# Optimization experiments

Measured on AMD Instinct MI355X. Metric: run time of the kernel, lower is better.

Reference implementation:

```python
import jax, jax.numpy as jnp
import numpy as np

DECAY = 0.99
EPS = 1e-05


def setup_inputs() -> dict:
    key = jax.random.key(0)
    k1, k2, k3, k4 = jax.random.split(key, 4)
    B, D, T, E = 16, 64, 4096, 1024
    x = jax.random.normal(k1, (B, D, T), dtype=jnp.float32)
    embedding = jax.random.uniform(k2, (E, D), dtype=jnp.float32,
                                   minval=-1.0 / E, maxval=1.0 / E)
    ema_size = jax.random.uniform(k3, (E,), dtype=jnp.float32)
    ema_w = jax.random.normal(k4, (D, E), dtype=jnp.float32)
    return {"x": x, "embedding": embedding, "ema_size": ema_size, "ema_w": ema_w}


def reference(x, embedding, ema_size, ema_w):
    # x: [B, D, T] (bdt_flag=True -> transpose to [B, T, D])
    B, D, T = x.shape
    E = embedding.shape[0]
    xt = jnp.swapaxes(x, 1, 2)                      # [B, T, D]
    flat = xt.reshape(-1, D)                        # [B*T, D]
    dist = (jnp.sum(embedding * embedding, axis=1)[None, :]
            - 2.0 * flat @ embedding.T
            + jnp.sum(flat * flat, axis=1, keepdims=True))  # [B*T, E]
    quantized_idx = jnp.argmin(dist, axis=1).reshape(B, T)   # [B, T] int
    onehot = jax.nn.one_hot(quantized_idx, E, dtype=x.dtype)  # [B, T, E]
    embed_idx = onehot @ embedding                  # [B, T, D]  (old codebook)
    # --- EMA codebook update (training branch) ---
    new_ema_size = DECAY * ema_size + (1.0 - DECAY) * jnp.sum(
        onehot.reshape(-1, E), axis=0)
    embed_sum = jnp.einsum('btd,bte->de', xt, onehot)        # [D, E]
    new_ema_w = DECAY * ema_w + (1.0 - DECAY) * embed_sum
    n = jnp.sum(new_ema_size)
    new_ema_size = (new_ema_size + EPS) / (n + E * EPS) * n
    new_embedding = (new_ema_w / new_ema_size[None, :]).T    # [E, D]
    # straight-through estimator
    embed_idx_qx = xt + jax.lax.stop_gradient(embed_idx - xt)
    embed_idx_qx = jnp.swapaxes(embed_idx_qx, 1, 2)          # back to [B, D, T]
    return embed_idx, embed_idx_qx, quantized_idx, new_embedding, new_ema_size, new_ema_w
```

## Files before the change

### kernel.cpp

```cpp
#include <hip/hip_runtime.h>
#include <hip/hip_bf16.h>

constexpr int Bc = 16, Dc = 64, Tc = 4096, Ec = 1024;
constexpr int NROW = Bc * Tc;
constexpr float DECAYF = 0.99f;
constexpr float OMDF   = 0.01f;
constexpr float EPSF   = 1e-5f;

typedef short bf16x8 __attribute__((ext_vector_type(8)));
typedef float f32x4  __attribute__((ext_vector_type(4)));

constexpr size_t O_EI  = 0;
constexpr size_t O_QX  = 4194304;
constexpr size_t O_IDX = 8388608;
constexpr size_t O_EMB = 8454144;
constexpr size_t O_ESZ = 8519680;
constexpr size_t O_EMW = 8520704;

constexpr size_t S_XH = 0;
constexpr size_t S_XM = 2097152;
constexpr size_t S_XL = 4194304;
constexpr size_t S_EH = 6291456;
constexpr size_t S_EM = 6324224;
constexpr size_t S_EL = 6356992;
constexpr size_t S_E2 = 6389760;
constexpr size_t S_X2 = 6424576;
constexpr size_t S_P  = 6557696;


__device__ inline unsigned short bf16bits(float v) {
  union { __hip_bfloat16 b; unsigned short u; } c;
  c.b = __float2bfloat16(v);
  return c.u;
}
__device__ inline float bf16val(unsigned short u) {
  union { unsigned u32; float f; } c;
  c.u32 = ((unsigned)u) << 16;
  return c.f;
}
__device__ inline void split3(float x, unsigned short& h, unsigned short& m,
                              unsigned short& l) {
  h = bf16bits(x);
  float r1 = x - bf16val(h);
  m = bf16bits(r1);
  float r2 = r1 - bf16val(m);
  l = bf16bits(r2);
}

__device__ inline void pack8(unsigned short* s, uint4* dst) {
  uint4 v;
  v.x = (unsigned)s[0] | ((unsigned)s[1] << 16);
  v.y = (unsigned)s[2] | ((unsigned)s[3] << 16);
  v.z = (unsigned)s[4] | ((unsigned)s[5] << 16);
  v.w = (unsigned)s[6] | ((unsigned)s[7] << 16);
  *dst = v;
}

__device__ inline void gl_lds16(const unsigned short* g, unsigned short* l) {
  __builtin_amdgcn_global_load_lds(
      (const __attribute__((address_space(1))) void*)g,
      (__attribute__((address_space(3))) void*)l, 16, 0, 0);
}

__global__ __launch_bounds__(256) void decomp_x(const float* __restrict__ x,
                                                float* __restrict__ out) {
  const int row = blockIdx.x * 256 + threadIdx.x;
  const int b = row >> 12, t = row & (Tc - 1);
  const float* xrow = x + (size_t)b * Dc * Tc + t;
  float xv[64];
  #pragma unroll
  for (int d = 0; d < Dc; ++d) xv[d] = xrow[(size_t)d * Tc];

  float x2;
  {
    #pragma clang fp contract(off)
    float r[8];
    #pragma unroll
    for (int j = 0; j < 8; ++j) r[j] = xv[j] * xv[j];
    #pragma unroll
    for (int k = 1; k < 8; ++k) {
      #pragma unroll
      for (int j = 0; j < 8; ++j) r[j] += xv[8 * k + j] * xv[8 * k + j];
    }
    x2 = ((r[0] + r[1]) + (r[2] + r[3])) + ((r[4] + r[5]) + (r[6] + r[7]));
  }
  out[S_X2 + row] = x2;

  uint4* ph = (uint4*)((unsigned short*)(out + S_XH) + (size_t)row * 64);
  uint4* pm = (uint4*)((unsigned short*)(out + S_XM) + (size_t)row * 64);
  uint4* pl = (uint4*)((unsigned short*)(out + S_XL) + (size_t)row * 64);
  #pragma unroll
  for (int k = 0; k < 8; ++k) {
    unsigned short hs[8], ms[8], ls[8];
    #pragma unroll
    for (int j = 0; j < 8; ++j) split3(xv[8 * k + j], hs[j], ms[j], ls[j]);
    pack8(hs, ph + k); pack8(ms, pm + k); pack8(ls, pl + k);
  }
}

__global__ __launch_bounds__(256) void decomp_e(const float* __restrict__ emb,
                                                float* __restrict__ out) {
  const int c = blockIdx.x * 256 + threadIdx.x;
  if (c >= Ec) return;
  const float* ep = emb + (size_t)c * Dc;
  float ev[64];
  #pragma unroll
  for (int d = 0; d < Dc; ++d) ev[d] = ep[d];

  float e2;
  {
    #pragma clang fp contract(off)
    float r[8];
    #pragma unroll
    for (int j = 0; j < 8; ++j) r[j] = ev[j] * ev[j];
    #pragma unroll
    for (int k = 1; k < 8; ++k) {
      #pragma unroll
      for (int j = 0; j < 8; ++j) r[j] += ev[8 * k + j] * ev[8 * k + j];
    }
    e2 = ((r[0] + r[1]) + (r[2] + r[3])) + ((r[4] + r[5]) + (r[6] + r[7]));
  }
  out[S_E2 + c] = e2;

  uint4* ph = (uint4*)((unsigned short*)(out + S_EH) + (size_t)c * 64);
  uint4* pm = (uint4*)((unsigned short*)(out + S_EM) + (size_t)c * 64);
  uint4* pl = (uint4*)((unsigned short*)(out + S_EL) + (size_t)c * 64);
  #pragma unroll
  for (int k = 0; k < 8; ++k) {
    unsigned short hs[8], ms[8], ls[8];
    #pragma unroll
    for (int j = 0; j < 8; ++j) split3(ev[8 * k + j], hs[j], ms[j], ls[j]);
    pack8(hs, ph + k); pack8(ms, pm + k); pack8(ls, pl + k);
  }
}

constexpr int TW = 64;
constexpr int SLOTS = (TW / 16) * 3 * 2 * 64;

__global__ __launch_bounds__(512)
__attribute__((amdgpu_waves_per_eu(2, 2)))
void gemm_argmin(float* __restrict__ out) {
  __shared__ alignas(16) unsigned short lbuf[2][SLOTS * 8];

  const int tid  = threadIdx.x;
  const int lane = tid & 63;
  const int wave = tid >> 6;
  const int col  = lane & 15;
  const int quad = lane >> 4;
  const int rowbase = blockIdx.x * 256 + wave * 32;

  const unsigned short* XH = (const unsigned short*)(out + S_XH);
  const unsigned short* XM = (const unsigned short*)(out + S_XM);
  const unsigned short* XL = (const unsigned short*)(out + S_XL);
  const unsigned short* EHu = (const unsigned short*)(out + S_EH);
  const float* E2 = out + S_E2;
  const float* X2 = out + S_X2;

  auto stage = [&](int tl, int s) {
    #pragma unroll
    for (int i = 0; i < 3; ++i) {
      int slot = tid + i * 512;
      int sl   = slot & 63;
      int sub  = slot >> 6;
      int half = sub & 1;
      int pl   = (sub >> 1) % 3;
      int nt   = sub / 6;
      int cw   = tl * TW + nt * 16 + (sl & 15);
      int q    = sl >> 4;
      const unsigned short* src =
          EHu + (size_t)pl * 65536 + (size_t)cw * 64 + half * 32 + q * 8;
      gl_lds16(src, &lbuf[s][(size_t)slot * 8]);
    }
  };

  bf16x8 a[12];
  #pragma unroll
  for (int mt = 0; mt < 2; ++mt) {
    size_t ao = (size_t)(rowbase + mt * 16 + col) * 64 + quad * 8;
    a[mt * 6 + 0] = *(const bf16x8*)(XH + ao);
    a[mt * 6 + 1] = *(const bf16x8*)(XH + ao + 32);
    a[mt * 6 + 2] = *(const bf16x8*)(XM + ao);
    a[mt * 6 + 3] = *(const bf16x8*)(XM + ao + 32);
    a[mt * 6 + 4] = *(const bf16x8*)(XL + ao);
    a[mt * 6 + 5] = *(const bf16x8*)(XL + ao + 32);
  }
  float x2v[8];
  #pragma unroll
  for (int mt = 0; mt < 2; ++mt)
    #pragma unroll
    for (int r = 0; r < 4; ++r)
      x2v[mt * 4 + r] = X2[rowbase + mt * 16 + quad * 4 + r];

  float best[8];
  int bidx[8];
  #pragma unroll
  for (int i = 0; i < 8; ++i) { best[i] = 3.4e38f; bidx[i] = 0; }

  stage(0, 0);

  for (int tl = 0; tl < Ec / TW; ++tl) {
    __syncthreads();
    if (tl + 1 < Ec / TW) stage(tl + 1, (tl + 1) & 1);
    const unsigned short* lb = lbuf[tl & 1];

    #pragma unroll
    for (int nt4 = 0; nt4 < TW / 16; ++nt4) {
      bf16x8 bb[6];
      #pragma unroll
      for (int pl = 0; pl < 3; ++pl)
        #pragma unroll
        for (int h = 0; h < 2; ++h)
          bb[pl * 2 + h] = *(const bf16x8*)(
              lb + ((size_t)(((nt4 * 3 + pl) * 2 + h) * 64 + lane)) * 8);
      const float e2v = E2[tl * TW + nt4 * 16 + col];

      f32x4 acc0 = {0.f, 0.f, 0.f, 0.f};
      f32x4 acc1 = {0.f, 0.f, 0.f, 0.f};
      const int PA[6] = {0, 0, 1, 1, 0, 2};
      const int PB[6] = {0, 1, 0, 1, 2, 0};
      #pragma unroll
      for (int p = 0; p < 6; ++p) {
        #pragma unroll
        for (int s = 0; s < 2; ++s) {
          bf16x8 bf = bb[PB[p] * 2 + s];
          acc0 = __builtin_amdgcn_mfma_f32_16x16x32_bf16(a[PA[p] * 2 + s], bf, acc0, 0, 0, 0);
          acc1 = __builtin_amdgcn_mfma_f32_16x16x32_bf16(a[6 + PA[p] * 2 + s], bf, acc1, 0, 0, 0);
        }
      }

      const int cwv = tl * TW + nt4 * 16 + col;
      #pragma unroll
      for (int r = 0; r < 4; ++r) {
        {
          float q = __builtin_fmaf(-2.0f, acc0[r], e2v);
          q = q + x2v[r];
          if (q < best[r]) { best[r] = q; bidx[r] = cwv; }
        }
        {
          float q = __builtin_fmaf(-2.0f, acc1[r], e2v);
          q = q + x2v[4 + r];
          if (q < best[4 + r]) { best[4 + r] = q; bidx[4 + r] = cwv; }
        }
      }
    }
  }

  #pragma unroll
  for (int i = 0; i < 8; ++i) {
    float bq = best[i];
    int bi = bidx[i];
    #pragma unroll
    for (int m = 1; m <= 8; m <<= 1) {
      float qo = __shfl_xor(bq, m, 64);
      int io = __shfl_xor(bi, m, 64);
      bool take = (qo < bq) || (qo == bq && io < bi);
      bq = take ? qo : bq;
      bi = take ? io : bi;
    }
    if (col == 0) {
      int mt = i >> 2, r = i & 3;
      int row = rowbase + mt * 16 + quad * 4 + r;
      out[O_IDX + row] = (float)bi;
    }
  }
}

__global__ __launch_bounds__(512) void esum_partial(float* __restrict__ out,
                                                    float* __restrict__ ws) {
  const int c = blockIdx.x;
  const int s = blockIdx.y;
  __shared__ float acc[4 * 1025];
  __shared__ float cnt[1024];
  for (int i = threadIdx.x; i < 4 * 1025; i += 512) acc[i] = 0.f;
  if (s == 0)
    for (int i = threadIdx.x; i < 1024; i += 512) cnt[i] = 0.f;
  __syncthreads();

  const unsigned short* XH = (const unsigned short*)(out + S_XH);
  const unsigned short* XM = (const unsigned short*)(out + S_XM);
  const unsigned short* XL = (const unsigned short*)(out + S_XL);

  #pragma unroll 2
  for (int it = 0; it < 8; ++it) {
    const int r = c * 4096 + it * 512 + threadIdx.x;
    const int bi = (int)out[O_IDX + r];
    const size_t off = (size_t)r * 64 + s * 4;
    const uint2 h = *(const uint2*)(XH + off);
    const uint2 m = *(const uint2*)(XM + off);
    const uint2 l = *(const uint2*)(XL + off);

#define DOPAIR(k, HW, MW, LW)                                                  \
    {                                                                          \
      float v0 = (bf16val((unsigned short)(HW)) +                              \
                  bf16val((unsigned short)(MW))) +                             \
                 bf16val((unsigned short)(LW));                                \
      float v1 = (bf16val((unsigned short)((HW) >> 16)) +                      \
                  bf16val((unsigned short)((MW) >> 16))) +                     \
                 bf16val((unsigned short)((LW) >> 16));                        \
      atomicAdd(&acc[(2 * (k) + 0) * 1025 + bi], v0);                          \
      atomicAdd(&acc[(2 * (k) + 1) * 1025 + bi], v1);                          \
    }
    DOPAIR(0, h.x, m.x, l.x)
    DOPAIR(1, h.y, m.y, l.y)
#undef DOPAIR
    if (s == 0) atomicAdd(&cnt[bi], 1.0f);
  }
  __syncthreads();

  float* part = out + S_P + ((size_t)c * 64 + s * 4) * 1024;
  for (int i = threadIdx.x; i < 4096; i += 512)
    part[i] = acc[(i >> 10) * 1025 + (i & 1023)];
  if (s == 0)
    for (int i = threadIdx.x; i < 1024; i += 512)
      atomicAdd(&ws[i], cnt[i]);
}

__global__ __launch_bounds__(256) void esum_reduce(const float* __restrict__ out,
                                                   float* __restrict__ ws) {
  const int i = blockIdx.x * 256 + threadIdx.x;
  float v = 0.f;
  #pragma unroll
  for (int c = 0; c < 16; ++c) v += out[S_P + (size_t)c * 65536 + i];
  ws[1024 + i] = v;
}

__global__ __launch_bounds__(256) void epilogue_kernel(
    const float* __restrict__ x, const float* __restrict__ emb,
    float* __restrict__ out) {
  const int row = blockIdx.x * 256 + threadIdx.x;
  const int b = row >> 12, t = row & (Tc - 1);
  const float* xrow = x + (size_t)b * Dc * Tc + t;

  const int bi = (int)out[O_IDX + row];

  const float4* eb = (const float4*)(emb + (size_t)bi * Dc);
  float* qx_base = out + O_QX + (size_t)b * Dc * Tc + t;
  float4* ei_base = (float4*)(out + O_EI + (size_t)row * Dc);

  #pragma unroll
  for (int k = 0; k < 16; ++k) {
    float4 ev = eb[k];
    ei_base[k] = ev;
    {
      const int d = 4 * k + 0; float xd = xrow[(size_t)d * Tc];
      float diff = ev.x - xd;
      qx_base[(size_t)d * Tc] = xd + diff;
    }
    {
      const int d = 4 * k + 1; float xd = xrow[(size_t)d * Tc];
      float diff = ev.y - xd;
      qx_base[(size_t)d * Tc] = xd + diff;
    }
    {
      const int d = 4 * k + 2; float xd = xrow[(size_t)d * Tc];
      float diff = ev.z - xd;
      qx_base[(size_t)d * Tc] = xd + diff;
    }
    {
      const int d = 4 * k + 3; float xd = xrow[(size_t)d * Tc];
      float diff = ev.w - xd;
      qx_base[(size_t)d * Tc] = xd + diff;
    }
  }
}

__global__ __launch_bounds__(1024) void finalize_a(
    const float* __restrict__ ema_size, float* __restrict__ ws,
    float* __restrict__ out) {
  const int e = threadIdx.x;
  float ns = DECAYF * ema_size[e] + OMDF * ws[e];
  __shared__ float red[1024];
  red[e] = ns;
  __syncthreads();
  for (int s = 512; s > 0; s >>= 1) {
    if (e < s) red[e] += red[e + s];
    __syncthreads();
  }
  float n = red[0];
  float v = ((ns + EPSF) / (n + (float)Ec * EPSF)) * n;
  out[O_ESZ + e] = v;
  ws[66560 + e] = v;
}

__global__ __launch_bounds__(256) void finalize_b(
    const float* __restrict__ ema_w, const float* __restrict__ ws,
    float* __restrict__ out) {
  int i = blockIdx.x * 256 + threadIdx.x;
  int d = i >> 10;
  int e = i & (Ec - 1);
  float w = DECAYF * ema_w[i] + OMDF * ws[1024 + i];
  out[O_EMW + i] = w;
  out[O_EMB + e * Dc + d] = w / ws[66560 + e];
}

extern "C" void kernel_launch(void* const* d_in, const int* in_sizes, int n_in,
                              void* d_out, int out_size, void* d_ws, size_t ws_size,
                              hipStream_t stream) {
  const float* x        = (const float*)d_in[0];
  const float* emb      = (const float*)d_in[1];
  const float* ema_size = (const float*)d_in[2];
  const float* ema_w    = (const float*)d_in[3];
  float* out = (float*)d_out;
  float* ws  = (float*)d_ws;

  (void)hipMemsetAsync(ws, 0, 1024 * sizeof(float), stream);
  decomp_x<<<NROW / 256, 256, 0, stream>>>(x, out);
  decomp_e<<<Ec / 256, 256, 0, stream>>>(emb, out);
  gemm_argmin<<<256, 512, 0, stream>>>(out);
  esum_partial<<<dim3(16, 16), 512, 0, stream>>>(out, ws);
  esum_reduce<<<NROW / 256, 256, 0, stream>>>(out, ws);
  epilogue_kernel<<<NROW / 256, 256, 0, stream>>>(x, emb, out);
  finalize_a<<<1, 1024, 0, stream>>>(ema_size, ws, out);
  finalize_b<<<Ec * Dc / 256, 256, 0, stream>>>(ema_w, ws, out);
}
```

Measured before the change: 192.6 us.

## Split codebook across wave halves in gemm_argmin and merge argmin via LDS

The GEMM+argmin kernel now processes 128 rows per block instead of 256. The two halves of the waves each scan half of the codebook (512 entries) with a smaller codeword tile, and their per-row minima are merged through shared memory. This doubles the grid to 512 blocks and raises the occupancy target to 4 waves per EU, improving latency hiding and CU fill on the 256-CU part. The cost is that each block re-reads the same A rows for half the work, and an extra barrier and LDS merge are added.

```diff
diff --git a/kernel.cpp b/kernel.cpp
--- a/kernel.cpp
+++ b/kernel.cpp
@@ -134,20 +134,24 @@
   }
 }
 
-constexpr int TW = 64;
+constexpr int TW = 32;
 constexpr int SLOTS = (TW / 16) * 3 * 2 * 64;
 
 __global__ __launch_bounds__(512)
-__attribute__((amdgpu_waves_per_eu(2, 2)))
+__attribute__((amdgpu_waves_per_eu(4, 4)))
 void gemm_argmin(float* __restrict__ out) {
-  __shared__ alignas(16) unsigned short lbuf[2][SLOTS * 8];
-
-  const int tid  = threadIdx.x;
-  const int lane = tid & 63;
-  const int wave = tid >> 6;
-  const int col  = lane & 15;
-  const int quad = lane >> 4;
-  const int rowbase = blockIdx.x * 256 + wave * 32;
+  __shared__ alignas(16) unsigned short lbuf[4][SLOTS * 8];
+  __shared__ float mq[4][4][8];
+  __shared__ int   mi[4][4][8];
+
+  const int tid    = threadIdx.x;
+  const int lane   = tid & 63;
+  const int wave   = tid >> 6;
+  const int rowgrp = wave & 3;
+  const int hN     = wave >> 2;
+  const int col    = lane & 15;
+  const int quad   = lane >> 4;
+  const int rowbase = blockIdx.x * 128 + rowgrp * 32;
 
   const unsigned short* XH = (const unsigned short*)(out + S_XH);
   const unsigned short* XM = (const unsigned short*)(out + S_XM);
@@ -156,20 +160,22 @@
   const float* E2 = out + S_E2;
   const float* X2 = out + S_X2;
 
-  auto stage = [&](int tl, int s) {
-    #pragma unroll
-    for (int i = 0; i < 3; ++i) {
+  auto stage = [&](int t, int s) {
+    #pragma unroll
+    for (int i = 0; i < 2; ++i) {
       int slot = tid + i * 512;
-      int sl   = slot & 63;
-      int sub  = slot >> 6;
-      int half = sub & 1;
-      int pl   = (sub >> 1) % 3;
-      int nt   = sub / 6;
-      int cw   = tl * TW + nt * 16 + (sl & 15);
-      int q    = sl >> 4;
-      const unsigned short* src =
-          EHu + (size_t)pl * 65536 + (size_t)cw * 64 + half * 32 + q * 8;
-      gl_lds16(src, &lbuf[s][(size_t)slot * 8]);
+      if (slot < SLOTS) {
+        int sl  = slot & 63;
+        int sub = slot >> 6;
+        int hf  = sub & 1;
+        int pl  = (sub >> 1) % 3;
+        int nt  = sub / 6;
+        int cw  = t * TW + nt * 16 + (sl & 15);
+        int q   = sl >> 4;
+        const unsigned short* src =
+            EHu + (size_t)pl * 65536 + (size_t)cw * 64 + hf * 32 + q * 8;
+        gl_lds16(src, &lbuf[s][(size_t)slot * 8]);
+      }
     }
   };
 
@@ -197,22 +203,27 @@
   for (int i = 0; i < 8; ++i) { best[i] = 3.4e38f; bidx[i] = 0; }
 
   stage(0, 0);
-
-  for (int tl = 0; tl < Ec / TW; ++tl) {
+  stage(16, 2);
+
+  for (int j = 0; j < 16; ++j) {
     __syncthreads();
-    if (tl + 1 < Ec / TW) stage(tl + 1, (tl + 1) & 1);
-    const unsigned short* lb = lbuf[tl & 1];
-
-    #pragma unroll
-    for (int nt4 = 0; nt4 < TW / 16; ++nt4) {
+    if (j + 1 < 16) {
+      stage(j + 1, (j + 1) & 1);
+      stage(16 + j + 1, 2 + ((j + 1) & 1));
+    }
+    const unsigned short* lb = lbuf[hN * 2 + (j & 1)];
+
+    #pragma unroll
+    for (int nt = 0; nt < 2; ++nt) {
       bf16x8 bb[6];
       #pragma unroll
       for (int pl = 0; pl < 3; ++pl)
         #pragma unroll
-        for (int h = 0; h < 2; ++h)
-          bb[pl * 2 + h] = *(const bf16x8*)(
-              lb + ((size_t)(((nt4 * 3 + pl) * 2 + h) * 64 + lane)) * 8);
-      const float e2v = E2[tl * TW + nt4 * 16 + col];
+        for (int hf = 0; hf < 2; ++hf)
+          bb[pl * 2 + hf] = *(const bf16x8*)(
+              lb + ((size_t)(((nt * 3 + pl) * 2 + hf) * 64 + lane)) * 8);
+      const int cwv = hN * 512 + j * TW + nt * 16 + col;
+      const float e2v = E2[cwv];
 
       f32x4 acc0 = {0.f, 0.f, 0.f, 0.f};
       f32x4 acc1 = {0.f, 0.f, 0.f, 0.f};
@@ -228,7 +239,6 @@
         }
       }
 
-      const int cwv = tl * TW + nt4 * 16 + col;
       #pragma unroll
       for (int r = 0; r < 4; ++r) {
         {
@@ -245,6 +255,8 @@
     }
   }
 
+  float fq[8];
+  int fi[8];
   #pragma unroll
   for (int i = 0; i < 8; ++i) {
     float bq = best[i];
@@ -257,10 +269,23 @@
       bq = take ? qo : bq;
       bi = take ? io : bi;
     }
-    if (col == 0) {
+    fq[i] = bq; fi[i] = bi;
+  }
+
+  if (hN == 1 && col == 0) {
+    #pragma unroll
+    for (int i = 0; i < 8; ++i) { mq[rowgrp][quad][i] = fq[i]; mi[rowgrp][quad][i] = fi[i]; }
+  }
+  __syncthreads();
+  if (hN == 0 && col == 0) {
+    #pragma unroll
+    for (int i = 0; i < 8; ++i) {
+      float q2 = mq[rowgrp][quad][i];
+      int i2 = mi[rowgrp][quad][i];
+      bool take = (q2 < fq[i]) || (q2 == fq[i] && i2 < fi[i]);
+      int bi = take ? i2 : fi[i];
       int mt = i >> 2, r = i & 3;
-      int row = rowbase + mt * 16 + quad * 4 + r;
-      out[O_IDX + row] = (float)bi;
+      out[O_IDX + rowbase + mt * 16 + quad * 4 + r] = (float)bi;
     }
   }
 }
@@ -406,7 +431,7 @@
   (void)hipMemsetAsync(ws, 0, 1024 * sizeof(float), stream);
   decomp_x<<<NROW / 256, 256, 0, stream>>>(x, out);
   decomp_e<<<Ec / 256, 256, 0, stream>>>(emb, out);
-  gemm_argmin<<<256, 512, 0, stream>>>(out);
+  gemm_argmin<<<NROW / 128, 512, 0, stream>>>(out);
   esum_partial<<<dim3(16, 16), 512, 0, stream>>>(out, ws);
   esum_reduce<<<NROW / 256, 256, 0, stream>>>(out, ws);
   epilogue_kernel<<<NROW / 256, 256, 0, stream>>>(x, emb, out);
```

Result: slower. 202.5 us (+5.2%).
